# Performance work log

Hardware: AMD Instinct MI355X
Metric: run time of the kernel (lower is better)

The kernel has to match this reference:

```python
import jax, jax.numpy as jnp
import numpy as np


def _lstm_dir(x, Wih, Whh, bih, bhh, reverse):
    """Single-direction LSTM. x: [T,B,Cin]; PyTorch gate order i,f,g,o."""
    T, B, _ = x.shape
    H = Whh.shape[1]
    # Precompute input-to-hidden GEMM for all timesteps at once: [T,B,4H]
    xg = jnp.einsum('tbc,gc->tbg', x, Wih) + (bih + bhh)

    def step(carry, xt):
        h, c = carry
        gates = xt + h @ Whh.T  # [B,4H]
        i, f, g, o = jnp.split(gates, 4, axis=-1)
        i = jax.nn.sigmoid(i)
        f = jax.nn.sigmoid(f)
        g = jnp.tanh(g)
        o = jax.nn.sigmoid(o)
        c = f * c + i * g
        h = o * jnp.tanh(c)
        return (h, c), h

    init = (jnp.zeros((B, H), x.dtype), jnp.zeros((B, H), x.dtype))
    _, hs = jax.lax.scan(step, init, xg, reverse=reverse)
    return hs  # [T,B,H], time-aligned with x for both directions


def _bilstm_layer(x, Wih_f, Whh_f, bih_f, bhh_f, Wih_b, Whh_b, bih_b, bhh_b):
    hf = _lstm_dir(x, Wih_f, Whh_f, bih_f, bhh_f, reverse=False)
    hb = _lstm_dir(x, Wih_b, Whh_b, bih_b, bhh_b, reverse=True)
    return jnp.concatenate([hf, hb], axis=-1)  # [T,B,2H]


def setup_inputs() -> dict:
    key = jax.random.key(0)
    ks = jax.random.split(key, 18)
    T, B, C, H = 160, 256, 512, 256
    G = 4 * H  # 1024
    s = 0.05  # small init to keep gates in the linear-ish regime
    inp = {"x": jax.random.normal(ks[0], (T, B, C), jnp.float32)}
    names = []
    for l, cin in ((0, C), (1, 2 * H)):
        for sfx in ("", "_reverse"):
            names.append((f"weight_ih_l{l}{sfx}", (G, cin)))
            names.append((f"weight_hh_l{l}{sfx}", (G, H)))
            names.append((f"bias_ih_l{l}{sfx}", (G,)))
            names.append((f"bias_hh_l{l}{sfx}", (G,)))
    for i, (nm, shp) in enumerate(names):
        inp[nm] = jax.random.normal(ks[i + 1], shp, jnp.float32) * s
    return inp


def reference(x,
              weight_ih_l0, weight_hh_l0, bias_ih_l0, bias_hh_l0,
              weight_ih_l0_reverse, weight_hh_l0_reverse, bias_ih_l0_reverse, bias_hh_l0_reverse,
              weight_ih_l1, weight_hh_l1, bias_ih_l1, bias_hh_l1,
              weight_ih_l1_reverse, weight_hh_l1_reverse, bias_ih_l1_reverse, bias_hh_l1_reverse):
    h0 = _bilstm_layer(x,
                       weight_ih_l0, weight_hh_l0, bias_ih_l0, bias_hh_l0,
                       weight_ih_l0_reverse, weight_hh_l0_reverse, bias_ih_l0_reverse, bias_hh_l0_reverse)
    h1 = _bilstm_layer(h0,
                       weight_ih_l1, weight_hh_l1, bias_ih_l1, bias_hh_l1,
                       weight_ih_l1_reverse, weight_hh_l1_reverse, bias_ih_l1_reverse, bias_hh_l1_reverse)
    return h1  # [T, B, 2H]
```

## Files before the change

### kernel.cpp

```cpp
#include <hip/hip_runtime.h>
#include <stdint.h>

typedef __attribute__((ext_vector_type(8))) short bf16x8;
typedef __attribute__((ext_vector_type(4))) float f32x4;

__device__ __forceinline__ float bf2f(unsigned short u) {
    union { unsigned int u32; float f; } v; v.u32 = ((unsigned int)u) << 16; return v.f;
}
__device__ __forceinline__ unsigned short f2bf(float f) {
    union { float f; unsigned int u32; } v; v.f = f;
    unsigned int r = v.u32 + 0x7FFFu + ((v.u32 >> 16) & 1u);
    return (unsigned short)(r >> 16);
}
__device__ __forceinline__ float sigm(float x) { return 1.f / (1.f + __expf(-x)); }
__device__ __forceinline__ float tanh_fast(float x) {
    float ax = fabsf(x);
    float e = __expf(-2.f * ax);
    float t = (1.f - e) / (1.f + e);
    return copysignf(t, x);
}

__global__ void f2bf_kernel(const float* __restrict__ src, unsigned short* __restrict__ dst, int n4) {
    int i = blockIdx.x * blockDim.x + threadIdx.x;
    if (i >= n4) return;
    float4 v = ((const float4*)src)[i];
    ushort4 o;
    o.x = f2bf(v.x); o.y = f2bf(v.y); o.z = f2bf(v.z); o.w = f2bf(v.w);
    ((ushort4*)dst)[i] = o;
}

__global__ void bias_comb_kernel(const float* __restrict__ bif, const float* __restrict__ bhf,
                                 const float* __restrict__ bir, const float* __restrict__ bhr,
                                 float* __restrict__ out) {
    int n = blockIdx.x * blockDim.x + threadIdx.x;
    if (n >= 2048) return;
    out[n] = (n < 1024) ? (bif[n] + bhf[n]) : (bir[n - 1024] + bhr[n - 1024]);
}

__global__ __launch_bounds__(256, 2) void gemm_bt_bias(
    const unsigned short* __restrict__ A, const unsigned short* __restrict__ B,
    const float* __restrict__ bias, unsigned short* __restrict__ C,
    int M, int N, int K) {
    const int bn0 = blockIdx.x * 128;
    const int bm0 = blockIdx.y * 128;
    const int tid = threadIdx.x;
    const int wave = tid >> 6, lane = tid & 63;
    const int ln15 = lane & 15, quad = lane >> 4;
    const int wr = wave >> 1, wc = wave & 1;

    __shared__ __align__(16) unsigned short At[128 * 72];
    __shared__ __align__(16) unsigned short Bt[128 * 72];

    f32x4 acc[4][4] = {};

    for (int ko = 0; ko < K; ko += 64) {
#pragma unroll
        for (int i = 0; i < 4; ++i) {
            int chunk = tid + i * 256;
            int row = chunk >> 3, cc = chunk & 7;
            *(bf16x8*)&At[row * 72 + cc * 8] = *(const bf16x8*)&A[(size_t)(bm0 + row) * K + ko + cc * 8];
            *(bf16x8*)&Bt[row * 72 + cc * 8] = *(const bf16x8*)&B[(size_t)(bn0 + row) * K + ko + cc * 8];
        }
        __syncthreads();
#pragma unroll
        for (int kk = 0; kk < 2; ++kk) {
            bf16x8 a[4], b[4];
#pragma unroll
            for (int f = 0; f < 4; ++f) {
                a[f] = *(const bf16x8*)&At[(wr * 64 + f * 16 + ln15) * 72 + kk * 32 + quad * 8];
                b[f] = *(const bf16x8*)&Bt[(wc * 64 + f * 16 + ln15) * 72 + kk * 32 + quad * 8];
            }
#pragma unroll
            for (int fi = 0; fi < 4; ++fi)
#pragma unroll
                for (int fj = 0; fj < 4; ++fj)
                    acc[fi][fj] = __builtin_amdgcn_mfma_f32_16x16x32_bf16(a[fi], b[fj], acc[fi][fj], 0, 0, 0);
        }
        __syncthreads();
    }
#pragma unroll
    for (int fi = 0; fi < 4; ++fi) {
        int row = bm0 + wr * 64 + fi * 16 + quad * 4;
#pragma unroll
        for (int fj = 0; fj < 4; ++fj) {
            int col = bn0 + wc * 64 + fj * 16 + ln15;
            float bv = bias[col];
#pragma unroll
            for (int r = 0; r < 4; ++r)
                C[(size_t)(row + r) * N + col] = f2bf(acc[fi][fj][r] + bv);
        }
    }
}

__global__ __launch_bounds__(256, 1) void lstm_scan3(
    const unsigned short* __restrict__ xg,
    const unsigned short* __restrict__ whh_f,
    const unsigned short* __restrict__ whh_r,
    unsigned short* __restrict__ out_bf,
    float* __restrict__ out_f,
    unsigned short* __restrict__ hexg,
    int* __restrict__ ctr)
{
    const int gid = blockIdx.x & 31;
    const int cg = blockIdx.x >> 5;
    const int dir = gid & 1, bg = gid >> 1;
    const int m0 = bg * 16;
    const int tid = threadIdx.x;
    const int wave = tid >> 6, lane = tid & 63;
    const int ln15 = lane & 15, quad = lane >> 4;
    const unsigned short* __restrict__ whh = dir ? whh_r : whh_f;
    int* __restrict__ cptr = ctr + (dir * 16 + bg) * 160;

    __shared__ float gbuf[16 * 260];

    bf16x8 Bfr[32];
#pragma unroll
    for (int kb = 0; kb < 8; ++kb)
#pragma unroll
        for (int nt = 0; nt < 4; ++nt)
            Bfr[kb * 4 + nt] = *(const bf16x8*)&whh[
                (size_t)(wave * 256 + cg * 64 + nt * 16 + ln15) * 256 + kb * 32 + quad * 8];

    const int cm = tid >> 4, cj = tid & 15;
    float c[4] = {0.f, 0.f, 0.f, 0.f};

    unsigned long long* hex64 = (unsigned long long*)hexg;

    for (int tt = 0; tt < 160; ++tt) {
        const int t = dir ? (159 - tt) : tt;

        f32x4 acc[4];
        {
            const unsigned short* xr = xg + (size_t)(t * 256 + m0 + quad * 4) * 2048
                                          + dir * 1024 + wave * 256 + cg * 64 + ln15;
#pragma unroll
            for (int nt = 0; nt < 4; ++nt)
#pragma unroll
                for (int r = 0; r < 4; ++r)
                    acc[nt][r] = bf2f(xr[(size_t)r * 2048 + nt * 16]);
        }

        if (tt > 0) {
            if (tid == 0) {
                int lim = 1 << 22;
                while (__hip_atomic_load(cptr + (tt - 1), __ATOMIC_RELAXED,
                                         __HIP_MEMORY_SCOPE_AGENT) < 4 && --lim) { }
            }
            __syncthreads();
        }

        const int slot_r = (tt + 1) & 1;
        unsigned long long* hsrc = hex64 + (size_t)((slot_r * 2 + dir) * 16 + bg) * 1024;
        bf16x8 af[8];
#pragma unroll
        for (int kb = 0; kb < 8; ++kb) {
            union { unsigned long long u[2]; bf16x8 v; } tm;
            unsigned long long* p = hsrc + ln15 * 64 + kb * 8 + quad * 2;
            tm.u[0] = __hip_atomic_load(p, __ATOMIC_RELAXED, __HIP_MEMORY_SCOPE_AGENT);
            tm.u[1] = __hip_atomic_load(p + 1, __ATOMIC_RELAXED, __HIP_MEMORY_SCOPE_AGENT);
            af[kb] = tm.v;
        }

#pragma unroll
        for (int kb = 0; kb < 8; ++kb)
#pragma unroll
            for (int nt = 0; nt < 4; ++nt)
                acc[nt] = __builtin_amdgcn_mfma_f32_16x16x32_bf16(af[kb], Bfr[kb * 4 + nt], acc[nt], 0, 0, 0);

#pragma unroll
        for (int nt = 0; nt < 4; ++nt)
#pragma unroll
            for (int r = 0; r < 4; ++r) {
                float v = acc[nt][r];
                v = (wave == 2) ? tanh_fast(v) : sigm(v);
                gbuf[(quad * 4 + r) * 260 + wave * 64 + nt * 16 + ln15] = v;
            }
        __syncthreads();

        const int slot_w = tt & 1;
        unsigned long long* hdst = hex64 + (size_t)((slot_w * 2 + dir) * 16 + bg) * 1024;
        const float* gb = gbuf + cm * 260;
        float hv[4];
#pragma unroll
        for (int p = 0; p < 4; ++p) {
            int jj = cg * 64 + cj * 4 + p;
            float iv = gb[jj];
            float fv = gb[256 + jj - 192];
            (void)iv; (void)fv;
            hv[p] = 0.f;
        }
#pragma unroll
        for (int p = 0; p < 4; ++p) {
            int lj = cj * 4 + p;
            float iv = gb[lj];
            float fv = gb[64 + lj];
            float gv = gb[128 + lj];
            float ov = gb[192 + lj];
            float cn = fv * c[p] + iv * gv;
            c[p] = cn;
            hv[p] = ov * tanh_fast(cn);
        }
        unsigned long long pk = (unsigned long long)f2bf(hv[0])
                              | ((unsigned long long)f2bf(hv[1]) << 16)
                              | ((unsigned long long)f2bf(hv[2]) << 32)
                              | ((unsigned long long)f2bf(hv[3]) << 48);
        __hip_atomic_store(hdst + cm * 64 + cg * 16 + cj, pk,
                           __ATOMIC_RELAXED, __HIP_MEMORY_SCOPE_AGENT);

        __syncthreads();
        if (tid == 0)
            __hip_atomic_fetch_add(cptr + tt, 1, __ATOMIC_RELAXED, __HIP_MEMORY_SCOPE_AGENT);

        size_t obase = (size_t)(t * 256 + m0 + cm) * 512 + dir * 256 + cg * 64 + cj * 4;
        if (out_f) {
            float4 o4; o4.x = hv[0]; o4.y = hv[1]; o4.z = hv[2]; o4.w = hv[3];
            *(float4*)&out_f[obase] = o4;
        } else {
            ushort4 o4;
            o4.x = f2bf(hv[0]); o4.y = f2bf(hv[1]); o4.z = f2bf(hv[2]); o4.w = f2bf(hv[3]);
            *(ushort4*)&out_bf[obase] = o4;
        }
    }
}

extern "C" void kernel_launch(void* const* d_in, const int* in_sizes, int n_in,
                              void* d_out, int out_size, void* d_ws, size_t ws_size,
                              hipStream_t stream) {
    const float* x = (const float*)d_in[0];
    float* out = (float*)d_out;
    char* ws = (char*)d_ws;

    unsigned short* xbf   = (unsigned short*)(ws + 0);
    unsigned short* wcat0 = (unsigned short*)(ws + 41943040LL);
    unsigned short* wcat1 = (unsigned short*)(ws + 44040192LL);
    unsigned short* whh0f = (unsigned short*)(ws + 46137344LL);
    unsigned short* whh0r = whh0f + 262144;
    unsigned short* whh1f = whh0f + 524288;
    unsigned short* whh1r = whh0f + 786432;
    float* bias0          = (float*)(ws + 48234496LL);
    float* bias1          = (float*)(ws + 48242688LL);
    unsigned short* xgbuf = (unsigned short*)(ws + 48250880LL);
    unsigned short* hexg  = (unsigned short*)(ws + 216023040LL);
    int* ctrbuf           = (int*)(ws + 216547328LL);
    unsigned short* h0b   = xbf;

    f2bf_kernel<<<20480, 256, 0, stream>>>(x, xbf, 5242880);
    f2bf_kernel<<<512, 256, 0, stream>>>((const float*)d_in[1], wcat0, 131072);
    f2bf_kernel<<<512, 256, 0, stream>>>((const float*)d_in[5], wcat0 + 524288, 131072);
    f2bf_kernel<<<512, 256, 0, stream>>>((const float*)d_in[9], wcat1, 131072);
    f2bf_kernel<<<512, 256, 0, stream>>>((const float*)d_in[13], wcat1 + 524288, 131072);
    f2bf_kernel<<<256, 256, 0, stream>>>((const float*)d_in[2], whh0f, 65536);
    f2bf_kernel<<<256, 256, 0, stream>>>((const float*)d_in[6], whh0r, 65536);
    f2bf_kernel<<<256, 256, 0, stream>>>((const float*)d_in[10], whh1f, 65536);
    f2bf_kernel<<<256, 256, 0, stream>>>((const float*)d_in[14], whh1r, 65536);
    bias_comb_kernel<<<8, 256, 0, stream>>>((const float*)d_in[3], (const float*)d_in[4],
                                            (const float*)d_in[7], (const float*)d_in[8], bias0);
    bias_comb_kernel<<<8, 256, 0, stream>>>((const float*)d_in[11], (const float*)d_in[12],
                                            (const float*)d_in[15], (const float*)d_in[16], bias1);

    dim3 gg(16, 320);
    gemm_bt_bias<<<gg, 256, 0, stream>>>(xbf, wcat0, bias0, xgbuf, 40960, 2048, 512);
    hipMemsetAsync(hexg, 0, 524288, stream);
    hipMemsetAsync(ctrbuf, 0, 20480, stream);
    lstm_scan3<<<128, 256, 0, stream>>>(xgbuf, whh0f, whh0r, h0b, nullptr, hexg, ctrbuf);
    gemm_bt_bias<<<gg, 256, 0, stream>>>(h0b, wcat1, bias1, xgbuf, 40960, 2048, 512);
    hipMemsetAsync(hexg, 0, 524288, stream);
    hipMemsetAsync(ctrbuf, 0, 20480, stream);
    lstm_scan3<<<128, 256, 0, stream>>>(xgbuf, whh1f, whh1r, nullptr, out, hexg, ctrbuf);
}
```

Baseline: 1.791 ms.

## Replace counter barrier with sentinel-flagged ring buffer for hidden-state exchange

The per-step cross-block handshake no longer uses an atomic counter that one thread polls. Each thread now polls the hidden-state words it needs directly, treating an all-ones sentinel as 'not yet written'. The exchange buffer becomes an 8-slot ring, and each step resets an older slot back to the sentinel. The gate shared buffer is double-buffered, which removes the trailing block barrier and the counter increment. This cuts a global atomic round trip and a __syncthreads from the serial per-step critical path, at the cost of more polling traffic, a larger ring (aliased onto the freed layer-0 weight buffer), and reliance on the sentinel never matching a real bf16 hidden-state pattern.

Result: faster. 1.743 ms (-2.7%).

```diff
diff --git a/kernel.cpp b/kernel.cpp
--- a/kernel.cpp
+++ b/kernel.cpp
@@ -92,14 +92,13 @@
     }
 }
 
-__global__ __launch_bounds__(256, 1) void lstm_scan3(
+__global__ __launch_bounds__(256, 1) void lstm_scan4(
     const unsigned short* __restrict__ xg,
     const unsigned short* __restrict__ whh_f,
     const unsigned short* __restrict__ whh_r,
     unsigned short* __restrict__ out_bf,
     float* __restrict__ out_f,
-    unsigned short* __restrict__ hexg,
-    int* __restrict__ ctr)
+    unsigned short* __restrict__ hexg)
 {
     const int gid = blockIdx.x & 31;
     const int cg = blockIdx.x >> 5;
@@ -109,9 +108,8 @@
     const int wave = tid >> 6, lane = tid & 63;
     const int ln15 = lane & 15, quad = lane >> 4;
     const unsigned short* __restrict__ whh = dir ? whh_r : whh_f;
-    int* __restrict__ cptr = ctr + (dir * 16 + bg) * 160;
-
-    __shared__ float gbuf[16 * 260];
+
+    __shared__ float gbuf[2][16 * 260];
 
     bf16x8 Bfr[32];
 #pragma unroll
@@ -125,6 +123,7 @@
     float c[4] = {0.f, 0.f, 0.f, 0.f};
 
     unsigned long long* hex64 = (unsigned long long*)hexg;
+    const unsigned long long SENT = ~0ull;
 
     for (int tt = 0; tt < 160; ++tt) {
         const int t = dir ? (159 - tt) : tt;
@@ -140,24 +139,38 @@
                     acc[nt][r] = bf2f(xr[(size_t)r * 2048 + nt * 16]);
         }
 
-        if (tt > 0) {
-            if (tid == 0) {
-                int lim = 1 << 22;
-                while (__hip_atomic_load(cptr + (tt - 1), __ATOMIC_RELAXED,
-                                         __HIP_MEMORY_SCOPE_AGENT) < 4 && --lim) { }
+        const int slot_r = (tt + 7) & 7;
+        unsigned long long* hsrc = hex64 + ((size_t)(slot_r * 2 + dir) * 16 + bg) * 1024
+                                 + ln15 * 64 + quad * 2;
+        unsigned long long w[16];
+        {
+            int lim = 1 << 20;
+            for (;;) {
+                bool ok = true;
+#pragma unroll
+                for (int kb = 0; kb < 8; ++kb) {
+                    w[kb * 2]     = __hip_atomic_load(hsrc + kb * 8,     __ATOMIC_RELAXED, __HIP_MEMORY_SCOPE_AGENT);
+                    w[kb * 2 + 1] = __hip_atomic_load(hsrc + kb * 8 + 1, __ATOMIC_RELAXED, __HIP_MEMORY_SCOPE_AGENT);
+                }
+#pragma unroll
+                for (int i = 0; i < 16; ++i) ok &= (w[i] != SENT);
+                if (ok || !--lim) break;
+                __builtin_amdgcn_s_sleep(2);
             }
-            __syncthreads();
-        }
-
-        const int slot_r = (tt + 1) & 1;
-        unsigned long long* hsrc = hex64 + (size_t)((slot_r * 2 + dir) * 16 + bg) * 1024;
+        }
+
+        {
+            const int slot_p = (tt + 6) & 7;
+            unsigned long long* pp = hex64 + ((size_t)(slot_p * 2 + dir) * 16 + bg) * 1024
+                                   + cm * 64 + cg * 16 + cj;
+            __hip_atomic_store(pp, SENT, __ATOMIC_RELAXED, __HIP_MEMORY_SCOPE_AGENT);
+        }
+
         bf16x8 af[8];
 #pragma unroll
         for (int kb = 0; kb < 8; ++kb) {
             union { unsigned long long u[2]; bf16x8 v; } tm;
-            unsigned long long* p = hsrc + ln15 * 64 + kb * 8 + quad * 2;
-            tm.u[0] = __hip_atomic_load(p, __ATOMIC_RELAXED, __HIP_MEMORY_SCOPE_AGENT);
-            tm.u[1] = __hip_atomic_load(p + 1, __ATOMIC_RELAXED, __HIP_MEMORY_SCOPE_AGENT);
+            tm.u[0] = w[kb * 2]; tm.u[1] = w[kb * 2 + 1];
             af[kb] = tm.v;
         }
 
@@ -167,28 +180,21 @@
             for (int nt = 0; nt < 4; ++nt)
                 acc[nt] = __builtin_amdgcn_mfma_f32_16x16x32_bf16(af[kb], Bfr[kb * 4 + nt], acc[nt], 0, 0, 0);
 
+        const int par = tt & 1;
 #pragma unroll
         for (int nt = 0; nt < 4; ++nt)
 #pragma unroll
             for (int r = 0; r < 4; ++r) {
                 float v = acc[nt][r];
                 v = (wave == 2) ? tanh_fast(v) : sigm(v);
-                gbuf[(quad * 4 + r) * 260 + wave * 64 + nt * 16 + ln15] = v;
+                gbuf[par][(quad * 4 + r) * 260 + wave * 64 + nt * 16 + ln15] = v;
             }
         __syncthreads();
 
-        const int slot_w = tt & 1;
-        unsigned long long* hdst = hex64 + (size_t)((slot_w * 2 + dir) * 16 + bg) * 1024;
-        const float* gb = gbuf + cm * 260;
+        const int slot_w = tt & 7;
+        unsigned long long* hdst = hex64 + ((size_t)(slot_w * 2 + dir) * 16 + bg) * 1024;
+        const float* gb = gbuf[par] + cm * 260;
         float hv[4];
-#pragma unroll
-        for (int p = 0; p < 4; ++p) {
-            int jj = cg * 64 + cj * 4 + p;
-            float iv = gb[jj];
-            float fv = gb[256 + jj - 192];
-            (void)iv; (void)fv;
-            hv[p] = 0.f;
-        }
 #pragma unroll
         for (int p = 0; p < 4; ++p) {
             int lj = cj * 4 + p;
@@ -206,10 +212,6 @@
                               | ((unsigned long long)f2bf(hv[3]) << 48);
         __hip_atomic_store(hdst + cm * 64 + cg * 16 + cj, pk,
                            __ATOMIC_RELAXED, __HIP_MEMORY_SCOPE_AGENT);
-
-        __syncthreads();
-        if (tid == 0)
-            __hip_atomic_fetch_add(cptr + tt, 1, __ATOMIC_RELAXED, __HIP_MEMORY_SCOPE_AGENT);
 
         size_t obase = (size_t)(t * 256 + m0 + cm) * 512 + dir * 256 + cg * 64 + cj * 4;
         if (out_f) {
@@ -240,8 +242,7 @@
     float* bias0          = (float*)(ws + 48234496LL);
     float* bias1          = (float*)(ws + 48242688LL);
     unsigned short* xgbuf = (unsigned short*)(ws + 48250880LL);
-    unsigned short* hexg  = (unsigned short*)(ws + 216023040LL);
-    int* ctrbuf           = (int*)(ws + 216547328LL);
+    unsigned short* hexg  = wcat0;
     unsigned short* h0b   = xbf;
 
     f2bf_kernel<<<20480, 256, 0, stream>>>(x, xbf, 5242880);
@@ -260,11 +261,11 @@
 
     dim3 gg(16, 320);
     gemm_bt_bias<<<gg, 256, 0, stream>>>(xbf, wcat0, bias0, xgbuf, 40960, 2048, 512);
-    hipMemsetAsync(hexg, 0, 524288, stream);
-    hipMemsetAsync(ctrbuf, 0, 20480, stream);
-    lstm_scan3<<<128, 256, 0, stream>>>(xgbuf, whh0f, whh0r, h0b, nullptr, hexg, ctrbuf);
+    hipMemsetAsync(hexg, 0xFF, 2097152, stream);
+    hipMemsetAsync((char*)hexg + 7 * 262144, 0, 262144, stream);
+    lstm_scan4<<<128, 256, 0, stream>>>(xgbuf, whh0f, whh0r, h0b, nullptr, hexg);
     gemm_bt_bias<<<gg, 256, 0, stream>>>(h0b, wcat1, bias1, xgbuf, 40960, 2048, 512);
-    hipMemsetAsync(hexg, 0, 524288, stream);
-    hipMemsetAsync(ctrbuf, 0, 20480, stream);
-    lstm_scan3<<<128, 256, 0, stream>>>(xgbuf, whh1f, whh1r, nullptr, out, hexg, ctrbuf);
-}
+    hipMemsetAsync(hexg, 0xFF, 2097152, stream);
+    hipMemsetAsync((char*)hexg + 7 * 262144, 0, 262144, stream);
+    lstm_scan4<<<128, 256, 0, stream>>>(xgbuf, whh1f, whh1r, nullptr, out, hexg);
+}
```
